# Kernel tuning notes

Measured on AMD Instinct MI355X. Metric: run time of the kernel, lower is better.

The kernel has to match this reference:

```python
import jax, jax.numpy as jnp
import numpy as np

B, CIN, COUT, H, W = 8, 128, 128, 64, 64
KH = KW = 3
STRIDE = PAD = 1
DIL = 1
K = KH * KW
EPS = 1e-4


def setup_inputs() -> dict:
    key = jax.random.key(0)
    k1, k2, k3 = jax.random.split(key, 3)
    Ho = (H + 2 * PAD - DIL * (KH - 1) - 1) // STRIDE + 1
    Wo = (W + 2 * PAD - DIL * (KW - 1) - 1) // STRIDE + 1
    x = jax.random.normal(k1, (B, CIN, H, W), dtype=jnp.float32)
    offset = jax.random.normal(k2, (B, 2 * K, Ho, Wo), dtype=jnp.float32)
    weight = jax.random.normal(k3, (COUT, CIN, KH, KW), dtype=jnp.float32) * 0.05
    return {"x": x, "offset": offset, "weight": weight}


def _bilinear_gather(x, py, px):
    # x: [B, C, H, W]; py/px: [B, K, Ho, Wo] float sampling positions
    Bn, C, Hn, Wn = x.shape
    x_flat = x.reshape(Bn, C, Hn * Wn)
    y0 = jnp.floor(py)
    x0 = jnp.floor(px)
    ly = py - y0  # fractional parts
    lx = px - x0
    out = 0.0
    corners = [(0.0, 0.0, (1 - ly) * (1 - lx)), (0.0, 1.0, (1 - ly) * lx),
               (1.0, 0.0, ly * (1 - lx)), (1.0, 1.0, ly * lx)]
    for dy, dx, wgt in corners:
        yy = y0 + dy
        xx = x0 + dx
        valid = (yy >= 0) & (yy < Hn) & (xx >= 0) & (xx < Wn)
        yi = jnp.clip(yy, 0, Hn - 1).astype(jnp.int32)
        xi = jnp.clip(xx, 0, Wn - 1).astype(jnp.int32)
        idx = (yi * Wn + xi).reshape(Bn, -1)  # [B, K*Ho*Wo]
        g = jax.vmap(lambda xf, ib: jnp.take(xf, ib, axis=1))(x_flat, idx)  # [B, C, N]
        out = out + g * (wgt * valid.astype(x.dtype)).reshape(Bn, 1, -1)
    return out  # [B, C, K*Ho*Wo]


def reference(x, offset, weight) -> jnp.ndarray:
    Bn = x.shape[0]
    Ho, Wo = offset.shape[2], offset.shape[3]
    # --- weight normalization (per output channel, per kernel tap) ---
    norm_fac = (KH * KW) ** 0.5
    length = jnp.sqrt(jnp.sum(jnp.square(weight) + EPS, axis=1, keepdims=True))  # [O,1,kh,kw]
    wn = weight / length / norm_fac  # [O, Cin, kh, kw]
    # --- sampling positions ---
    off = offset.reshape(Bn, K, 2, Ho, Wo)
    off_y, off_x = off[:, :, 0], off[:, :, 1]
    ky, kx = jnp.meshgrid(jnp.arange(KH), jnp.arange(KW), indexing="ij")
    ky = (ky.reshape(K) * DIL).astype(jnp.float32)
    kx = (kx.reshape(K) * DIL).astype(jnp.float32)
    base_y = (jnp.arange(Ho) * STRIDE - PAD).astype(jnp.float32)
    base_x = (jnp.arange(Wo) * STRIDE - PAD).astype(jnp.float32)
    py = base_y[None, None, :, None] + ky[None, :, None, None] + off_y  # [B,K,Ho,Wo]
    px = base_x[None, None, None, :] + kx[None, :, None, None] + off_x
    # --- deformable im2col + GEMM ---
    cols = _bilinear_gather(x, py, px).reshape(Bn, CIN, K, Ho, Wo)
    out = jnp.einsum("bckhw,ock->bohw", cols, wn.reshape(COUT, CIN, K))
    return out
```

## Files before the change

kernel.cpp:

```cpp
#include <hip/hip_runtime.h>
#include <hip/hip_bf16.h>
#include <hip/hip_fp16.h>
#include <math.h>


typedef __attribute__((ext_vector_type(8))) short short8;
typedef __attribute__((ext_vector_type(4))) float floatx4;
typedef __attribute__((ext_vector_type(2))) float floatx2;

static __device__ __forceinline__ unsigned int f2bf(float f) {
    unsigned int u = __float_as_uint(f);
    u += 0x7fffu + ((u >> 16) & 1u);
    return u >> 16;
}
static __device__ __forceinline__ unsigned int packbf2(float lo, float hi) {
    __hip_bfloat162 h = __float22bfloat162_rn(make_float2(lo, hi));
    unsigned int u;
    __builtin_memcpy(&u, &h, 4);
    return u;
}
static __device__ __forceinline__ floatx2 bf2f2(unsigned int w) {
    floatx2 r;
    r.x = __uint_as_float(w << 16);
    r.y = __uint_as_float(w & 0xffff0000u);
    return r;
}

__global__ void prep_k(const float* __restrict__ x, const float* __restrict__ w,
                       unsigned int* __restrict__ xt32, unsigned short* __restrict__ wb) {
    __shared__ float lds[128 * 65];
    const int tid = threadIdx.x;

    if (blockIdx.x < 512) {
        const int b = blockIdx.x & 7, h = (blockIdx.x >> 3) & 63;
        const float* xp = x + (b * 128 * 64 + h) * 64;
        #pragma unroll 4
        for (int i = 0; i < 32; i++) {
            const int c = i * 4 + (tid >> 6);
            const int ww = tid & 63;
            lds[c * 65 + ww] = xp[c * 4096 + ww];
        }
        __syncthreads();
        unsigned int* xo = xt32 + (b * 64 + h) * 4096;
        #pragma unroll 4
        for (int i = 0; i < 16; i++) {
            const int flat2 = i * 256 + tid;
            const int ww = flat2 >> 6, cp = flat2 & 63;
            xo[flat2] = packbf2(lds[(2 * cp) * 65 + ww], lds[(2 * cp + 1) * 65 + ww]);
        }
    } else {
        const int o = (blockIdx.x - 512) * 4 + (tid >> 6);
        const int lane = tid & 63;
        const float* wo = w + o * 1152;
        float v[18];
        #pragma unroll
        for (int i = 0; i < 18; i++) v[i] = wo[lane * 18 + i];
        float s[9];
        #pragma unroll
        for (int k = 0; k < 9; k++) s[k] = v[k] * v[k] + v[9 + k] * v[9 + k];
        #pragma unroll
        for (int d = 32; d >= 1; d >>= 1) {
            #pragma unroll
            for (int k = 0; k < 9; k++) s[k] += __shfl_xor(s[k], d, 64);
        }
        const int c0 = 2 * lane, c1 = c0 + 1;
        #pragma unroll
        for (int k = 0; k < 9; k++) {
            const float inv = 1.0f / (3.0f * sqrtf(s[k] + 0.0128f));
            wb[((k * 16 + (c0 >> 3)) * 128 + o) * 8 + (c0 & 7)] = (unsigned short)f2bf(v[k] * inv);
            wb[((k * 16 + (c1 >> 3)) * 128 + o) * 8 + (c1 & 7)] = (unsigned short)f2bf(v[9 + k] * inv);
        }
    }
}

static __device__ __forceinline__ unsigned int bl1(const float4 w,
                                                   unsigned int r0, unsigned int r1,
                                                   unsigned int r2, unsigned int r3) {
    floatx2 a = bf2f2(r0) * w.x;
    a += bf2f2(r1) * w.y;
    a += bf2f2(r2) * w.z;
    a += bf2f2(r3) * w.w;
    return packbf2(a.x, a.y);
}

static __device__ __forceinline__ uint4 combine4(const float4 wvv,
                                                 const uint4 r0, const uint4 r1,
                                                 const uint4 r2, const uint4 r3) {
    uint4 pk;
    pk.x = bl1(wvv, r0.x, r1.x, r2.x, r3.x);
    pk.y = bl1(wvv, r0.y, r1.y, r2.y, r3.y);
    pk.z = bl1(wvv, r0.z, r1.z, r2.z, r3.z);
    pk.w = bl1(wvv, r0.w, r1.w, r2.w, r3.w);
    return pk;
}

static __device__ __forceinline__ void rec_expand(const uint4 rec, float4& wvv, int4& iv) {
    const float2 w01 = __half22float2(*reinterpret_cast<const __half2*>(&rec.x));
    const float2 w23 = __half22float2(*reinterpret_cast<const __half2*>(&rec.y));
    wvv = make_float4(w01.x, w01.y, w23.x, w23.y);
    iv = make_int4((int)(rec.z & 0xffffu) << 7, (int)(rec.z >> 16) << 7,
                   (int)(rec.w & 0xffffu) << 7, (int)(rec.w >> 16) << 7);
}

static __device__ __forceinline__ void lds_barrier() {
    asm volatile("s_waitcnt lgkmcnt(0)" ::: "memory");
    __builtin_amdgcn_s_barrier();
    asm volatile("" ::: "memory");
}

__global__ __launch_bounds__(256, 4) void dconv_k(
    const unsigned short* __restrict__ xt, const float* __restrict__ off,
    const unsigned short* __restrict__ wb, float* __restrict__ out)
{
    __shared__ alignas(16) uint4 tapG[288];
    __shared__ alignas(16) unsigned short colsS[2][16 * 264];

    const int idx = blockIdx.x;
    const int b = idx & 7;
    const int half = (idx >> 3) & 1;
    const int ho = (idx >> 4) & 63;
    const int tid = threadIdx.x;
    const int wbase = half * 32;

    for (int t = tid; t < 288; t += 256) {
        const int k = t >> 5, p = t & 31;
        const int wg = wbase + p;
        const int oidx = ((b * 18 + 2 * k) * 64 + ho) * 64 + wg;
        const float offy = off[oidx];
        const float offx = off[oidx + 4096];
        const float py = (float)(ho - 1 + (k / 3)) + offy;
        const float px = (float)(wg - 1 + (k % 3)) + offx;
        const float y0f = floorf(py), x0f = floorf(px);
        const float ly = py - y0f, lx = px - x0f;
        const int y0 = (int)y0f, x0 = (int)x0f;
        const int y1 = y0 + 1, x1 = x0 + 1;
        const float fy0 = (y0 >= 0 && y0 < 64) ? (1.0f - ly) : 0.0f;
        const float fy1 = (y1 >= 0 && y1 < 64) ? ly : 0.0f;
        const float fx0 = (x0 >= 0 && x0 < 64) ? (1.0f - lx) : 0.0f;
        const float fx1 = (x1 >= 0 && x1 < 64) ? lx : 0.0f;
        const int yc0 = min(max(y0, 0), 63), yc1 = min(max(y1, 0), 63);
        const int xc0 = min(max(x0, 0), 63), xc1 = min(max(x1, 0), 63);
        const __half2 a01 = __float22half2_rn(make_float2(fy0 * fx0, fy0 * fx1));
        const __half2 a23 = __float22half2_rn(make_float2(fy1 * fx0, fy1 * fx1));
        uint4 pk;
        __builtin_memcpy(&pk.x, &a01, 4);
        __builtin_memcpy(&pk.y, &a23, 4);
        pk.z = (unsigned int)(yc0 * 64 + xc0) | ((unsigned int)(yc0 * 64 + xc1) << 16);
        pk.w = (unsigned int)(yc1 * 64 + xc0) | ((unsigned int)(yc1 * 64 + xc1) << 16);
        tapG[t] = pk;
    }
    __syncthreads();

    const int lane = tid & 63, wv = tid >> 6;
    const int quad = lane >> 4, l16 = lane & 15;
    const int g = tid & 15, p0 = tid >> 4;
    const unsigned short* xb = xt + b * (64 * 64 * 128);
    const int obase = wv * 32;

    floatx4 acc[4];
    #pragma unroll
    for (int t = 0; t < 4; t++) acc[t] = (floatx4)0.0f;

    uint4 r[2][4];
    float4 wvv[2];

    #pragma unroll
    for (int i = 0; i < 2; i++) {
        const int p = p0 + i * 16;
        float4 w0; int4 iv;
        rec_expand(tapG[p], w0, iv);
        const uint4 c0 = *(const uint4*)(xb + iv.x + g * 8);
        const uint4 c1 = *(const uint4*)(xb + iv.y + g * 8);
        const uint4 c2 = *(const uint4*)(xb + iv.z + g * 8);
        const uint4 c3 = *(const uint4*)(xb + iv.w + g * 8);
        *(uint4*)&colsS[0][g * 264 + p * 8] = combine4(w0, c0, c1, c2, c3);
    }
    #pragma unroll
    for (int i = 0; i < 2; i++) {
        const int p = p0 + i * 16;
        int4 iv;
        rec_expand(tapG[32 + p], wvv[i], iv);
        r[i][0] = *(const uint4*)(xb + iv.x + g * 8);
        r[i][1] = *(const uint4*)(xb + iv.y + g * 8);
        r[i][2] = *(const uint4*)(xb + iv.z + g * 8);
        r[i][3] = *(const uint4*)(xb + iv.w + g * 8);
    }
    lds_barrier();

    for (int k = 0; k < 9; k++) {
        const int cur = k & 1;

        const unsigned short* wk = wb + k * 16384;
        short8 a[8];
        #pragma unroll
        for (int q = 0; q < 4; q++) {
            const int cgrp = q * 4 + quad;
            #pragma unroll
            for (int n = 0; n < 2; n++)
                a[q * 2 + n] = *(const short8*)(wk + (cgrp * 128 + obase + n * 16 + l16) * 8);
        }

        if (k < 8) {
            #pragma unroll
            for (int i = 0; i < 2; i++) {
                const int p = p0 + i * 16;
                *(uint4*)&colsS[cur ^ 1][g * 264 + p * 8] =
                    combine4(wvv[i], r[i][0], r[i][1], r[i][2], r[i][3]);
            }
        }

        if (k < 7) {
            #pragma unroll
            for (int i = 0; i < 2; i++) {
                const int p = p0 + i * 16;
                int4 iv;
                rec_expand(tapG[(k + 2) * 32 + p], wvv[i], iv);
                r[i][0] = *(const uint4*)(xb + iv.x + g * 8);
                r[i][1] = *(const uint4*)(xb + iv.y + g * 8);
                r[i][2] = *(const uint4*)(xb + iv.z + g * 8);
                r[i][3] = *(const uint4*)(xb + iv.w + g * 8);
            }
        }

        #pragma unroll
        for (int q = 0; q < 4; q++) {
            const int cgrp = q * 4 + quad;
            const short8 bf0 = *(const short8*)&colsS[cur][cgrp * 264 + l16 * 8];
            const short8 bf1 = *(const short8*)&colsS[cur][cgrp * 264 + (16 + l16) * 8];
            acc[0] = __builtin_amdgcn_mfma_f32_16x16x32_bf16(a[q * 2 + 0], bf0, acc[0], 0, 0, 0);
            acc[1] = __builtin_amdgcn_mfma_f32_16x16x32_bf16(a[q * 2 + 1], bf0, acc[1], 0, 0, 0);
            acc[2] = __builtin_amdgcn_mfma_f32_16x16x32_bf16(a[q * 2 + 0], bf1, acc[2], 0, 0, 0);
            acc[3] = __builtin_amdgcn_mfma_f32_16x16x32_bf16(a[q * 2 + 1], bf1, acc[3], 0, 0, 0);
        }

        if (k < 8) lds_barrier();
    }

    float* ob = out + b * 128 * 4096 + ho * 64 + wbase;
    #pragma unroll
    for (int t = 0; t < 2; t++) {
        const int pix = t * 16 + l16;
        #pragma unroll
        for (int n = 0; n < 2; n++) {
            #pragma unroll
            for (int r2 = 0; r2 < 4; r2++) {
                __builtin_nontemporal_store(acc[t * 2 + n][r2],
                    &ob[(obase + n * 16 + quad * 4 + r2) * 4096 + pix]);
            }
        }
    }
}

extern "C" void kernel_launch(void* const* d_in, const int* in_sizes, int n_in,
                              void* d_out, int out_size, void* d_ws, size_t ws_size,
                              hipStream_t stream) {
    const float* x   = (const float*)d_in[0];
    const float* off = (const float*)d_in[1];
    const float* w   = (const float*)d_in[2];
    float* out = (float*)d_out;

    unsigned short* xt = (unsigned short*)d_ws;
    unsigned short* wbuf = xt + 8 * 64 * 64 * 128;

    hipLaunchKernelGGL(prep_k,  dim3(544), dim3(256), 0, stream,
                       x, w, (unsigned int*)xt, wbuf);
    hipLaunchKernelGGL(dconv_k, dim3(1024), dim3(256), 0, stream, xt, off, wbuf, out);
}
```

Baseline: 96.68 us.

## Fuse prep and deformable conv into one cooperative kernel with grid sync

Merges the bf16 transpose and weight normalization prep into the conv kernel and launches it cooperatively, with a grid-wide barrier between the two phases. Each of the 1024 blocks transposes half the channels for one (b,h) row, and the first 128 blocks also normalize one output channel's weights. The goal is to remove the second kernel launch and the gap between kernels. In exchange it adds a grid sync, more LDS per block (which may lower occupancy), and falls back to the two-kernel path if the cooperative launch fails.

```diff
diff --git a/kernel.cpp b/kernel.cpp
--- a/kernel.cpp
+++ b/kernel.cpp
@@ -1,7 +1,10 @@
 #include <hip/hip_runtime.h>
+#include <hip/hip_cooperative_groups.h>
 #include <hip/hip_bf16.h>
 #include <hip/hip_fp16.h>
 #include <math.h>
+
+namespace cg = cooperative_groups;
 
 
 typedef __attribute__((ext_vector_type(8))) short short8;
@@ -24,53 +27,6 @@
     r.x = __uint_as_float(w << 16);
     r.y = __uint_as_float(w & 0xffff0000u);
     return r;
-}
-
-__global__ void prep_k(const float* __restrict__ x, const float* __restrict__ w,
-                       unsigned int* __restrict__ xt32, unsigned short* __restrict__ wb) {
-    __shared__ float lds[128 * 65];
-    const int tid = threadIdx.x;
-
-    if (blockIdx.x < 512) {
-        const int b = blockIdx.x & 7, h = (blockIdx.x >> 3) & 63;
-        const float* xp = x + (b * 128 * 64 + h) * 64;
-        #pragma unroll 4
-        for (int i = 0; i < 32; i++) {
-            const int c = i * 4 + (tid >> 6);
-            const int ww = tid & 63;
-            lds[c * 65 + ww] = xp[c * 4096 + ww];
-        }
-        __syncthreads();
-        unsigned int* xo = xt32 + (b * 64 + h) * 4096;
-        #pragma unroll 4
-        for (int i = 0; i < 16; i++) {
-            const int flat2 = i * 256 + tid;
-            const int ww = flat2 >> 6, cp = flat2 & 63;
-            xo[flat2] = packbf2(lds[(2 * cp) * 65 + ww], lds[(2 * cp + 1) * 65 + ww]);
-        }
-    } else {
-        const int o = (blockIdx.x - 512) * 4 + (tid >> 6);
-        const int lane = tid & 63;
-        const float* wo = w + o * 1152;
-        float v[18];
-        #pragma unroll
-        for (int i = 0; i < 18; i++) v[i] = wo[lane * 18 + i];
-        float s[9];
-        #pragma unroll
-        for (int k = 0; k < 9; k++) s[k] = v[k] * v[k] + v[9 + k] * v[9 + k];
-        #pragma unroll
-        for (int d = 32; d >= 1; d >>= 1) {
-            #pragma unroll
-            for (int k = 0; k < 9; k++) s[k] += __shfl_xor(s[k], d, 64);
-        }
-        const int c0 = 2 * lane, c1 = c0 + 1;
-        #pragma unroll
-        for (int k = 0; k < 9; k++) {
-            const float inv = 1.0f / (3.0f * sqrtf(s[k] + 0.0128f));
-            wb[((k * 16 + (c0 >> 3)) * 128 + o) * 8 + (c0 & 7)] = (unsigned short)f2bf(v[k] * inv);
-            wb[((k * 16 + (c1 >> 3)) * 128 + o) * 8 + (c1 & 7)] = (unsigned short)f2bf(v[9 + k] * inv);
-        }
-    }
 }
 
 static __device__ __forceinline__ unsigned int bl1(const float4 w,
@@ -108,18 +64,69 @@
     asm volatile("" ::: "memory");
 }
 
-__global__ __launch_bounds__(256, 4) void dconv_k(
-    const unsigned short* __restrict__ xt, const float* __restrict__ off,
-    const unsigned short* __restrict__ wb, float* __restrict__ out)
+static __device__ __forceinline__ void wnorm_one(const float* __restrict__ w,
+                                                 unsigned short* __restrict__ wb,
+                                                 int o, int lane) {
+    const float* wo = w + o * 1152;
+    float v[18];
+    #pragma unroll
+    for (int i = 0; i < 18; i++) v[i] = wo[lane * 18 + i];
+    float s[9];
+    #pragma unroll
+    for (int k = 0; k < 9; k++) s[k] = v[k] * v[k] + v[9 + k] * v[9 + k];
+    #pragma unroll
+    for (int d = 32; d >= 1; d >>= 1) {
+        #pragma unroll
+        for (int k = 0; k < 9; k++) s[k] += __shfl_xor(s[k], d, 64);
+    }
+    const int c0 = 2 * lane, c1 = c0 + 1;
+    #pragma unroll
+    for (int k = 0; k < 9; k++) {
+        const float inv = 1.0f / (3.0f * sqrtf(s[k] + 0.0128f));
+        wb[((k * 16 + (c0 >> 3)) * 128 + o) * 8 + (c0 & 7)] = (unsigned short)f2bf(v[k] * inv);
+        wb[((k * 16 + (c1 >> 3)) * 128 + o) * 8 + (c1 & 7)] = (unsigned short)f2bf(v[9 + k] * inv);
+    }
+}
+
+__global__ __launch_bounds__(256, 4) void fused_k(
+    const float* __restrict__ x, const float* __restrict__ off,
+    const float* __restrict__ w, unsigned int* __restrict__ xt32,
+    unsigned short* __restrict__ wb, float* __restrict__ out)
 {
+    __shared__ float tlds[64 * 65];
     __shared__ alignas(16) uint4 tapG[288];
     __shared__ alignas(16) unsigned short colsS[2][16 * 264];
 
     const int idx = blockIdx.x;
+    const int tid = threadIdx.x;
+
+    {
+        const int b = idx & 7, h = (idx >> 3) & 63, chalf = (idx >> 9) & 1;
+        const float* xp = x + (((b * 128 + chalf * 64) * 64) + h) * 64;
+        #pragma unroll 4
+        for (int i = 0; i < 16; i++) {
+            const int c = i * 4 + (tid >> 6);
+            const int ww = tid & 63;
+            tlds[c * 65 + ww] = xp[c * 4096 + ww];
+        }
+        __syncthreads();
+        unsigned int* xo = xt32 + (b * 64 + h) * 4096;
+        #pragma unroll 4
+        for (int i = 0; i < 8; i++) {
+            const int flat2 = i * 256 + tid;
+            const int ww = flat2 >> 5, cp = flat2 & 31;
+            xo[ww * 64 + chalf * 32 + cp] =
+                packbf2(tlds[(2 * cp) * 65 + ww], tlds[(2 * cp + 1) * 65 + ww]);
+        }
+        if (idx < 128 && tid < 64) wnorm_one(w, wb, idx, tid);
+    }
+
+    __threadfence();
+    cg::this_grid().sync();
+
     const int b = idx & 7;
     const int half = (idx >> 3) & 1;
     const int ho = (idx >> 4) & 63;
-    const int tid = threadIdx.x;
     const int wbase = half * 32;
 
     for (int t = tid; t < 288; t += 256) {
@@ -154,7 +161,7 @@
     const int lane = tid & 63, wv = tid >> 6;
     const int quad = lane >> 4, l16 = lane & 15;
     const int g = tid & 15, p0 = tid >> 4;
-    const unsigned short* xb = xt + b * (64 * 64 * 128);
+    const unsigned short* xb = (const unsigned short*)xt32 + b * (64 * 64 * 128);
     const int obase = wv * 32;
 
     floatx4 acc[4];
@@ -190,7 +197,7 @@
     for (int k = 0; k < 9; k++) {
         const int cur = k & 1;
 
-        const unsigned short* wk = wb + k * 16384;
+        const unsigned short* wk = (const unsigned short*)wb + k * 16384;
         short8 a[8];
         #pragma unroll
         for (int q = 0; q < 4; q++) {
@@ -251,6 +258,172 @@
     }
 }
 
+__global__ void prep_k(const float* __restrict__ x, const float* __restrict__ w,
+                       unsigned int* __restrict__ xt32, unsigned short* __restrict__ wb) {
+    __shared__ float lds[128 * 65];
+    const int tid = threadIdx.x;
+
+    if (blockIdx.x < 512) {
+        const int b = blockIdx.x & 7, h = (blockIdx.x >> 3) & 63;
+        const float* xp = x + (b * 128 * 64 + h) * 64;
+        #pragma unroll 4
+        for (int i = 0; i < 32; i++) {
+            const int c = i * 4 + (tid >> 6);
+            const int ww = tid & 63;
+            lds[c * 65 + ww] = xp[c * 4096 + ww];
+        }
+        __syncthreads();
+        unsigned int* xo = xt32 + (b * 64 + h) * 4096;
+        #pragma unroll 4
+        for (int i = 0; i < 16; i++) {
+            const int flat2 = i * 256 + tid;
+            const int ww = flat2 >> 6, cp = flat2 & 63;
+            xo[flat2] = packbf2(lds[(2 * cp) * 65 + ww], lds[(2 * cp + 1) * 65 + ww]);
+        }
+    } else {
+        const int o = (blockIdx.x - 512) * 4 + (tid >> 6);
+        wnorm_one(w, wb, o, tid & 63);
+    }
+}
+
+__global__ __launch_bounds__(256, 4) void dconv_k(
+    const unsigned short* __restrict__ xt, const float* __restrict__ off,
+    const unsigned short* __restrict__ wb, float* __restrict__ out)
+{
+    __shared__ alignas(16) uint4 tapG[288];
+    __shared__ alignas(16) unsigned short colsS[2][16 * 264];
+
+    const int idx = blockIdx.x;
+    const int b = idx & 7;
+    const int half = (idx >> 3) & 1;
+    const int ho = (idx >> 4) & 63;
+    const int tid = threadIdx.x;
+    const int wbase = half * 32;
+
+    for (int t = tid; t < 288; t += 256) {
+        const int k = t >> 5, p = t & 31;
+        const int wg = wbase + p;
+        const int oidx = ((b * 18 + 2 * k) * 64 + ho) * 64 + wg;
+        const float offy = off[oidx];
+        const float offx = off[oidx + 4096];
+        const float py = (float)(ho - 1 + (k / 3)) + offy;
+        const float px = (float)(wg - 1 + (k % 3)) + offx;
+        const float y0f = floorf(py), x0f = floorf(px);
+        const float ly = py - y0f, lx = px - x0f;
+        const int y0 = (int)y0f, x0 = (int)x0f;
+        const int y1 = y0 + 1, x1 = x0 + 1;
+        const float fy0 = (y0 >= 0 && y0 < 64) ? (1.0f - ly) : 0.0f;
+        const float fy1 = (y1 >= 0 && y1 < 64) ? ly : 0.0f;
+        const float fx0 = (x0 >= 0 && x0 < 64) ? (1.0f - lx) : 0.0f;
+        const float fx1 = (x1 >= 0 && x1 < 64) ? lx : 0.0f;
+        const int yc0 = min(max(y0, 0), 63), yc1 = min(max(y1, 0), 63);
+        const int xc0 = min(max(x0, 0), 63), xc1 = min(max(x1, 0), 63);
+        const __half2 a01 = __float22half2_rn(make_float2(fy0 * fx0, fy0 * fx1));
+        const __half2 a23 = __float22half2_rn(make_float2(fy1 * fx0, fy1 * fx1));
+        uint4 pk;
+        __builtin_memcpy(&pk.x, &a01, 4);
+        __builtin_memcpy(&pk.y, &a23, 4);
+        pk.z = (unsigned int)(yc0 * 64 + xc0) | ((unsigned int)(yc0 * 64 + xc1) << 16);
+        pk.w = (unsigned int)(yc1 * 64 + xc0) | ((unsigned int)(yc1 * 64 + xc1) << 16);
+        tapG[t] = pk;
+    }
+    __syncthreads();
+
+    const int lane = tid & 63, wv = tid >> 6;
+    const int quad = lane >> 4, l16 = lane & 15;
+    const int g = tid & 15, p0 = tid >> 4;
+    const unsigned short* xb = xt + b * (64 * 64 * 128);
+    const int obase = wv * 32;
+
+    floatx4 acc[4];
+    #pragma unroll
+    for (int t = 0; t < 4; t++) acc[t] = (floatx4)0.0f;
+
+    uint4 r[2][4];
+    float4 wvv[2];
+
+    #pragma unroll
+    for (int i = 0; i < 2; i++) {
+        const int p = p0 + i * 16;
+        float4 w0; int4 iv;
+        rec_expand(tapG[p], w0, iv);
+        const uint4 c0 = *(const uint4*)(xb + iv.x + g * 8);
+        const uint4 c1 = *(const uint4*)(xb + iv.y + g * 8);
+        const uint4 c2 = *(const uint4*)(xb + iv.z + g * 8);
+        const uint4 c3 = *(const uint4*)(xb + iv.w + g * 8);
+        *(uint4*)&colsS[0][g * 264 + p * 8] = combine4(w0, c0, c1, c2, c3);
+    }
+    #pragma unroll
+    for (int i = 0; i < 2; i++) {
+        const int p = p0 + i * 16;
+        int4 iv;
+        rec_expand(tapG[32 + p], wvv[i], iv);
+        r[i][0] = *(const uint4*)(xb + iv.x + g * 8);
+        r[i][1] = *(const uint4*)(xb + iv.y + g * 8);
+        r[i][2] = *(const uint4*)(xb + iv.z + g * 8);
+        r[i][3] = *(const uint4*)(xb + iv.w + g * 8);
+    }
+    lds_barrier();
+
+    for (int k = 0; k < 9; k++) {
+        const int cur = k & 1;
+        const unsigned short* wk = wb + k * 16384;
+        short8 a[8];
+        #pragma unroll
+        for (int q = 0; q < 4; q++) {
+            const int cgrp = q * 4 + quad;
+            #pragma unroll
+            for (int n = 0; n < 2; n++)
+                a[q * 2 + n] = *(const short8*)(wk + (cgrp * 128 + obase + n * 16 + l16) * 8);
+        }
+        if (k < 8) {
+            #pragma unroll
+            for (int i = 0; i < 2; i++) {
+                const int p = p0 + i * 16;
+                *(uint4*)&colsS[cur ^ 1][g * 264 + p * 8] =
+                    combine4(wvv[i], r[i][0], r[i][1], r[i][2], r[i][3]);
+            }
+        }
+        if (k < 7) {
+            #pragma unroll
+            for (int i = 0; i < 2; i++) {
+                const int p = p0 + i * 16;
+                int4 iv;
+                rec_expand(tapG[(k + 2) * 32 + p], wvv[i], iv);
+                r[i][0] = *(const uint4*)(xb + iv.x + g * 8);
+                r[i][1] = *(const uint4*)(xb + iv.y + g * 8);
+                r[i][2] = *(const uint4*)(xb + iv.z + g * 8);
+                r[i][3] = *(const uint4*)(xb + iv.w + g * 8);
+            }
+        }
+        #pragma unroll
+        for (int q = 0; q < 4; q++) {
+            const int cgrp = q * 4 + quad;
+            const short8 bf0 = *(const short8*)&colsS[cur][cgrp * 264 + l16 * 8];
+            const short8 bf1 = *(const short8*)&colsS[cur][cgrp * 264 + (16 + l16) * 8];
+            acc[0] = __builtin_amdgcn_mfma_f32_16x16x32_bf16(a[q * 2 + 0], bf0, acc[0], 0, 0, 0);
+            acc[1] = __builtin_amdgcn_mfma_f32_16x16x32_bf16(a[q * 2 + 1], bf0, acc[1], 0, 0, 0);
+            acc[2] = __builtin_amdgcn_mfma_f32_16x16x32_bf16(a[q * 2 + 0], bf1, acc[2], 0, 0, 0);
+            acc[3] = __builtin_amdgcn_mfma_f32_16x16x32_bf16(a[q * 2 + 1], bf1, acc[3], 0, 0, 0);
+        }
+        if (k < 8) lds_barrier();
+    }
+
+    float* ob = out + b * 128 * 4096 + ho * 64 + wbase;
+    #pragma unroll
+    for (int t = 0; t < 2; t++) {
+        const int pix = t * 16 + l16;
+        #pragma unroll
+        for (int n = 0; n < 2; n++) {
+            #pragma unroll
+            for (int r2 = 0; r2 < 4; r2++) {
+                __builtin_nontemporal_store(acc[t * 2 + n][r2],
+                    &ob[(obase + n * 16 + quad * 4 + r2) * 4096 + pix]);
+            }
+        }
+    }
+}
+
 extern "C" void kernel_launch(void* const* d_in, const int* in_sizes, int n_in,
                               void* d_out, int out_size, void* d_ws, size_t ws_size,
                               hipStream_t stream) {
@@ -261,8 +434,16 @@
 
     unsigned short* xt = (unsigned short*)d_ws;
     unsigned short* wbuf = xt + 8 * 64 * 64 * 128;
-
-    hipLaunchKernelGGL(prep_k,  dim3(544), dim3(256), 0, stream,
-                       x, w, (unsigned int*)xt, wbuf);
-    hipLaunchKernelGGL(dconv_k, dim3(1024), dim3(256), 0, stream, xt, off, wbuf, out);
-}
+    unsigned int* xt32 = (unsigned int*)xt;
+
+    void* args[] = { (void*)&x, (void*)&off, (void*)&w,
+                     (void*)&xt32, (void*)&wbuf, (void*)&out };
+    hipError_t e = hipLaunchCooperativeKernel(fused_k, dim3(1024), dim3(256),
+                                              args, 0u, stream);
+    if (e != hipSuccess) {
+        hipLaunchKernelGGL(prep_k,  dim3(544), dim3(256), 0, stream,
+                           x, w, xt32, wbuf);
+        hipLaunchKernelGGL(dconv_k, dim3(1024), dim3(256), 0, stream,
+                           xt, off, wbuf, out);
+    }
+}
```

Result: slower. 260.2 us (+169.1%).
